# Kernel optimization log

Hardware: AMD Instinct MI355X
Metric: run time of the kernel (lower is better)

The kernel has to match this reference:

```python
import jax, jax.numpy as jnp
import numpy as np

S = 2048      # total tokens
DIM = 1024    # model dim
H = 16        # attention heads
DH = 64       # head dim
BOT = 256     # bottleneck dim
NIMG = 4      # images (equal size)
L = S // NIMG # tokens per image
K = 256       # sparse_k
IH = 4        # indexer heads
ID = 16       # indexer head dim
MAXREL = 64   # hardcoded in module
NBUCK = 2 * MAXREL + 1
GH = IH * 2   # gate MLP hidden (expansion=2)


def setup_inputs() -> dict:
    key = jax.random.key(0)
    ks = jax.random.split(key, 16)
    r = lambda i, sh, s=0.02: jax.random.normal(ks[i], sh, jnp.float32) * s
    return dict(
        hidden_states=jax.random.normal(ks[0], (S, DIM), jnp.float32),
        patch_coords=jax.random.randint(ks[1], (S, 2), 0, 64, dtype=jnp.int32),
        cu_seqlens=jnp.arange(NIMG + 1, dtype=jnp.int32) * L,
        rotary_pos_emb=jax.random.uniform(ks[2], (S, DH // 2), jnp.float32) * 3.0,
        Wq_idx=r(3, (2 * IH * ID, DIM)),
        Wk_idx=r(4, (2 * IH * ID, DIM)),
        W1g=r(5, (GH, IH)), b1g=jnp.zeros((GH,), jnp.float32),
        W2g=r(6, (IH, GH)), b2g=jnp.zeros((IH,), jnp.float32),
        rpe_table=r(7, (NBUCK, IH)),
        Wqkv_d=r(8, (BOT, DIM)), bqkv_d=jnp.zeros((BOT,), jnp.float32),
        Wqkv_u=r(9, (3 * DIM, BOT)), bqkv_u=jnp.zeros((3 * DIM,), jnp.float32),
        Wp_d=r(10, (BOT, DIM)), bp_d=jnp.zeros((BOT,), jnp.float32),
        Wp_u=r(11, (DIM, BOT)), bp_u=jnp.zeros((DIM,), jnp.float32),
        scaler=jnp.ones((1,), jnp.float32),
    )


def _rotate_half(x):
    x1, x2 = jnp.split(x, 2, axis=-1)
    return jnp.concatenate([-x2, x1], axis=-1)


def reference(hidden_states, patch_coords, cu_seqlens, rotary_pos_emb,
              Wq_idx, Wk_idx, W1g, b1g, W2g, b2g, rpe_table,
              Wqkv_d, bqkv_d, Wqkv_u, bqkv_u, Wp_d, bp_d, Wp_u, bp_u, scaler):
    n = cu_seqlens.shape[0] - 1            # images (equal size L)
    Li = hidden_states.shape[0] // n
    neg = jnp.finfo(hidden_states.dtype).min

    # QKV via low-rank bottleneck
    qkv = (hidden_states @ Wqkv_d.T + bqkv_d) @ Wqkv_u.T + bqkv_u  # [S, 3*DIM]
    qkv = qkv.reshape(S, 3, H, DH)
    q, k, v = qkv[:, 0], qkv[:, 1], qkv[:, 2]                      # [S, H, DH]

    # vision RoPE (emb = cat(rpe, rpe))
    emb = jnp.concatenate([rotary_pos_emb, rotary_pos_emb], axis=-1)  # [S, DH]
    cos = jnp.cos(emb)[:, None, :]
    sin = jnpp if False else jnp.sin(emb)[:, None, :]
    q = q * cos + _rotate_half(q) * sin
    k = k * cos + _rotate_half(k) * sin

    # ---- interaction indexer, vmapped over equal-size images ----
    xs = hidden_states.reshape(n, Li, DIM)
    pos = patch_coords[:, 1].reshape(n, Li).astype(jnp.float32)
    qI = (xs @ Wq_idx.T).reshape(n, Li, 2 * IH, ID)
    kI = (xs @ Wk_idx.T).reshape(n, Li, 2 * IH, ID)
    dot = jnp.einsum('nqhd,nkhd->nqkh', qI, kI)                    # [n, L, L, 2*IH]
    data_in, gate_in = dot[..., :IH], dot[..., IH:]
    rel = jnp.clip(pos[:, :, None] - pos[:, None, :], -MAXREL, MAXREL)
    bucket = (rel + MAXREL).astype(jnp.int32)                      # [n, L, L]
    rpe = rpe_table[bucket]                                        # [n, L, L, IH]
    relu_scores = jax.nn.relu(data_in + rpe)
    g = jax.nn.sigmoid(jax.nn.relu((gate_in + rpe) @ W1g.T + b1g) @ W2g.T + b2g)
    index_scores = (relu_scores * g).sum(-1)                       # [n, L, L]

    # top-k sparse mask (0 at selected keys, -inf-ish elsewhere)
    _, topk_idx = jax.lax.top_k(index_scores, K)                   # [n, L, K]
    ni = jnp.arange(n)[:, None, None]
    ri = jnp.arange(Li)[None, :, None]
    mask_local = jnp.full((n, Li, Li), neg, hidden_states.dtype).at[ni, ri, topk_idx].set(0.0)

    # block-diagonal full mask
    mask = jnp.full((S, S), neg, hidden_states.dtype)
    for i in range(n):
        mask = mask.at[i * Li:(i + 1) * Li, i * Li:(i + 1) * Li].set(mask_local[i])

    # dense SDPA with additive mask
    att = jnp.einsum('qhd,khd->hqk', q, k) / jnp.sqrt(jnp.float32(DH)).astype(q.dtype)
    att = att + mask[None]
    p = jax.nn.softmax(att, axis=-1)
    out = jnp.einsum('hqk,khd->qhd', p, v).reshape(S, H * DH)

    final = (out @ Wp_d.T + bp_d) @ Wp_u.T + bp_u
    return final * scaler
```

## Files before the change

### kernel.cpp

```cpp
#include <hip/hip_runtime.h>
#include <hip/hip_bf16.h>

#define S_    2048
#define DIM_  1024
#define H_    16
#define DH_   64
#define BOT_  256
#define NIMG_ 4
#define LI_   512
#define K_    256
#define IH_   4
#define ID_   16
#define MAXREL_ 64
#define NBUCK_ 129
#define GH_   8
#define IDH2_ 128

typedef short bf16x8 __attribute__((ext_vector_type(8)));
typedef float f32x4  __attribute__((ext_vector_type(4)));

__device__ __forceinline__ unsigned short f2bf(float x) {
    unsigned u = __float_as_uint(x);
    return (unsigned short)((u + 0x7fffu + ((u >> 16) & 1u)) >> 16);
}
__device__ __forceinline__ float bf2f(unsigned short h) {
    return __uint_as_float(((unsigned)h) << 16);
}

#define OFF_W1_    2097152
#define OFF_WQ_    2359296
#define OFF_WK_    2490368
#define OFF_WQKVU_ 2621440
#define OFF_WPD_   3407872
#define OFF_WPU_   3670016
#define NSPLIT_    3932160

__global__ __launch_bounds__(256) void split_all_kernel(
    const float* __restrict__ hid, const float* __restrict__ wqd,
    const float* __restrict__ wq,  const float* __restrict__ wk,
    const float* __restrict__ wqu, const float* __restrict__ wpd,
    const float* __restrict__ wpu,
    unsigned short* __restrict__ hi, unsigned short* __restrict__ lo)
{
    long e = ((long)blockIdx.x * 256 + threadIdx.x) * 4;
    if (e >= NSPLIT_) return;
    const float* src; long off;
    if (e < OFF_W1_)         { src = hid; off = 0; }
    else if (e < OFF_WQ_)    { src = wqd; off = OFF_W1_; }
    else if (e < OFF_WK_)    { src = wq;  off = OFF_WQ_; }
    else if (e < OFF_WQKVU_) { src = wk;  off = OFF_WK_; }
    else if (e < OFF_WPD_)   { src = wqu; off = OFF_WQKVU_; }
    else if (e < OFF_WPU_)   { src = wpd; off = OFF_WPD_; }
    else                     { src = wpu; off = OFF_WPU_; }
    float4 v = *(const float4*)(src + (e - off));
    ushort4 h, l;
    h.x = f2bf(v.x); l.x = f2bf(v.x - bf2f(h.x));
    h.y = f2bf(v.y); l.y = f2bf(v.y - bf2f(h.y));
    h.z = f2bf(v.z); l.z = f2bf(v.z - bf2f(h.z));
    h.w = f2bf(v.w); l.w = f2bf(v.w - bf2f(h.w));
    *(ushort4*)&hi[e] = h;
    *(ushort4*)&lo[e] = l;
}

__global__ __launch_bounds__(256) void gemm_bf16x3(
    const unsigned short* __restrict__ Ah, const unsigned short* __restrict__ Al,
    const unsigned short* __restrict__ Bh, const unsigned short* __restrict__ Bl,
    const float* __restrict__ bias, const float* __restrict__ scale_ptr,
    float* __restrict__ Cf, int M, int N, int Kd)
{
    __shared__ unsigned short sAh[128 * 40], sAl[128 * 40];
    __shared__ unsigned short sBh[64 * 40],  sBl[64 * 40];
    int tid = threadIdx.x;
    int lane = tid & 63, wv = tid >> 6;
    int wr = wv >> 1, wc = wv & 1;
    int row0 = blockIdx.y * 128, col0 = blockIdx.x * 64;

    f32x4 acc[4][2];
#pragma unroll
    for (int i = 0; i < 4; i++)
#pragma unroll
        for (int j = 0; j < 2; j++) acc[i][j] = (f32x4){0.f, 0.f, 0.f, 0.f};

    int ar = tid >> 1, ac = (tid & 1) * 16;
    int br = tid >> 2, bc = (tid & 3) * 8;
    const unsigned short* gAh = Ah + (size_t)(row0 + ar) * Kd + ac;
    const unsigned short* gAl = Al + (size_t)(row0 + ar) * Kd + ac;
    const unsigned short* gBh = Bh + (size_t)(col0 + br) * Kd + bc;
    const unsigned short* gBl = Bl + (size_t)(col0 + br) * Kd + bc;
    int am = lane & 15, qk = (lane >> 4) * 8;

    for (int k0 = 0; k0 < Kd; k0 += 32) {
        __syncthreads();
        *(float4*)&sAh[ar * 40 + ac]     = *(const float4*)(gAh + k0);
        *(float4*)&sAh[ar * 40 + ac + 8] = *(const float4*)(gAh + k0 + 8);
        *(float4*)&sAl[ar * 40 + ac]     = *(const float4*)(gAl + k0);
        *(float4*)&sAl[ar * 40 + ac + 8] = *(const float4*)(gAl + k0 + 8);
        *(float4*)&sBh[br * 40 + bc]     = *(const float4*)(gBh + k0);
        *(float4*)&sBl[br * 40 + bc]     = *(const float4*)(gBl + k0);
        __syncthreads();

        bf16x8 ah[4], al[4], bh[2], bl[2];
#pragma unroll
        for (int rt = 0; rt < 4; rt++) {
            int r = wr * 64 + rt * 16 + am;
            ah[rt] = *(const bf16x8*)&sAh[r * 40 + qk];
            al[rt] = *(const bf16x8*)&sAl[r * 40 + qk];
        }
#pragma unroll
        for (int ct = 0; ct < 2; ct++) {
            int c = wc * 32 + ct * 16 + am;
            bh[ct] = *(const bf16x8*)&sBh[c * 40 + qk];
            bl[ct] = *(const bf16x8*)&sBl[c * 40 + qk];
        }
#pragma unroll
        for (int rt = 0; rt < 4; rt++)
#pragma unroll
            for (int ct = 0; ct < 2; ct++) {
                acc[rt][ct] = __builtin_amdgcn_mfma_f32_16x16x32_bf16(ah[rt], bh[ct], acc[rt][ct], 0, 0, 0);
                acc[rt][ct] = __builtin_amdgcn_mfma_f32_16x16x32_bf16(ah[rt], bl[ct], acc[rt][ct], 0, 0, 0);
                acc[rt][ct] = __builtin_amdgcn_mfma_f32_16x16x32_bf16(al[rt], bh[ct], acc[rt][ct], 0, 0, 0);
            }
    }

    float scl = scale_ptr ? *scale_ptr : 1.0f;
    int rq = (lane >> 4) * 4;
#pragma unroll
    for (int rt = 0; rt < 4; rt++)
#pragma unroll
        for (int ct = 0; ct < 2; ct++) {
            int col = col0 + wc * 32 + ct * 16 + am;
            float bz = bias ? bias[col] : 0.0f;
#pragma unroll
            for (int rg = 0; rg < 4; rg++) {
                int row = row0 + wr * 64 + rt * 16 + rq + rg;
                Cf[(size_t)row * N + col] = (acc[rt][ct][rg] + bz) * scl;
            }
        }
}

__global__ __launch_bounds__(256) void gemm64_bf16x3(
    const unsigned short* __restrict__ Ah, const unsigned short* __restrict__ Al,
    const unsigned short* __restrict__ Bh, const unsigned short* __restrict__ Bl,
    const float* __restrict__ bias_lo, const float* __restrict__ bias_hi,
    float* __restrict__ Cf, unsigned short* __restrict__ Chi,
    unsigned short* __restrict__ Clo, int M, int N, int Kd, int split_col)
{
    __shared__ unsigned short sAh[64 * 72], sAl[64 * 72];
    __shared__ unsigned short sBh[64 * 72], sBl[64 * 72];
    int tid = threadIdx.x;
    int lane = tid & 63, wv = tid >> 6;
    int wr = wv >> 1, wc = wv & 1;
    int row0 = blockIdx.y * 64, col0 = blockIdx.x * 64;

    f32x4 acc[2][2];
#pragma unroll
    for (int i = 0; i < 2; i++)
#pragma unroll
        for (int j = 0; j < 2; j++) acc[i][j] = (f32x4){0.f, 0.f, 0.f, 0.f};

    int sr = tid >> 2, sc = (tid & 3) * 16;
    const unsigned short* gAh = Ah + (size_t)(row0 + sr) * Kd + sc;
    const unsigned short* gAl = Al + (size_t)(row0 + sr) * Kd + sc;
    const unsigned short* gBh = Bh + (size_t)(col0 + sr) * Kd + sc;
    const unsigned short* gBl = Bl + (size_t)(col0 + sr) * Kd + sc;
    int am = lane & 15, qk = (lane >> 4) * 8;

    for (int k0 = 0; k0 < Kd; k0 += 64) {
        __syncthreads();
        *(float4*)&sAh[sr * 72 + sc]     = *(const float4*)(gAh + k0);
        *(float4*)&sAh[sr * 72 + sc + 8] = *(const float4*)(gAh + k0 + 8);
        *(float4*)&sAl[sr * 72 + sc]     = *(const float4*)(gAl + k0);
        *(float4*)&sAl[sr * 72 + sc + 8] = *(const float4*)(gAl + k0 + 8);
        *(float4*)&sBh[sr * 72 + sc]     = *(const float4*)(gBh + k0);
        *(float4*)&sBh[sr * 72 + sc + 8] = *(const float4*)(gBh + k0 + 8);
        *(float4*)&sBl[sr * 72 + sc]     = *(const float4*)(gBl + k0);
        *(float4*)&sBl[sr * 72 + sc + 8] = *(const float4*)(gBl + k0 + 8);
        __syncthreads();

#pragma unroll
        for (int ks = 0; ks < 2; ks++) {
            bf16x8 ah[2], al[2], bh[2], bl[2];
#pragma unroll
            for (int rt = 0; rt < 2; rt++) {
                int r = wr * 32 + rt * 16 + am;
                ah[rt] = *(const bf16x8*)&sAh[r * 72 + ks * 32 + qk];
                al[rt] = *(const bf16x8*)&sAl[r * 72 + ks * 32 + qk];
            }
#pragma unroll
            for (int ct = 0; ct < 2; ct++) {
                int c = wc * 32 + ct * 16 + am;
                bh[ct] = *(const bf16x8*)&sBh[c * 72 + ks * 32 + qk];
                bl[ct] = *(const bf16x8*)&sBl[c * 72 + ks * 32 + qk];
            }
#pragma unroll
            for (int rt = 0; rt < 2; rt++)
#pragma unroll
                for (int ct = 0; ct < 2; ct++) {
                    acc[rt][ct] = __builtin_amdgcn_mfma_f32_16x16x32_bf16(ah[rt], bh[ct], acc[rt][ct], 0, 0, 0);
                    acc[rt][ct] = __builtin_amdgcn_mfma_f32_16x16x32_bf16(ah[rt], bl[ct], acc[rt][ct], 0, 0, 0);
                    acc[rt][ct] = __builtin_amdgcn_mfma_f32_16x16x32_bf16(al[rt], bh[ct], acc[rt][ct], 0, 0, 0);
                }
        }
    }

    int rq = (lane >> 4) * 4;
#pragma unroll
    for (int rt = 0; rt < 2; rt++)
#pragma unroll
        for (int ct = 0; ct < 2; ct++) {
            int col = col0 + wc * 32 + ct * 16 + am;
#pragma unroll
            for (int rg = 0; rg < 4; rg++) {
                int row = row0 + wr * 32 + rt * 16 + rq + rg;
                float v = acc[rt][ct][rg];
                if (col < split_col) {
                    if (bias_lo) v += bias_lo[col];
                    size_t idx = (size_t)row * split_col + col;
                    unsigned short hh = f2bf(v);
                    Chi[idx] = hh;
                    Clo[idx] = f2bf(v - bf2f(hh));
                } else {
                    if (bias_hi) v += bias_hi[col - split_col];
                    Cf[(size_t)row * (N - split_col) + col - split_col] = v;
                }
            }
        }
}

__global__ __launch_bounds__(256) void rope_kernel(
    float* __restrict__ qkv, const float* __restrict__ rope)
{
    int idx = blockIdx.x * blockDim.x + threadIdx.x;
    if (idx >= S_ * H_ * 32) return;
    int d = idx & 31;
    int h = (idx >> 5) & (H_ - 1);
    int s = idx >> 9;
    float r = rope[s * 32 + d];
    float c = cosf(r), sn = sinf(r);
    size_t base = (size_t)s * 3072 + h * 64 + d;
    float q1 = qkv[base], q2 = qkv[base + 32];
    qkv[base]      = q1 * c - q2 * sn;
    qkv[base + 32] = q2 * c + q1 * sn;
    float k1 = qkv[base + 1024], k2 = qkv[base + 1024 + 32];
    qkv[base + 1024]      = k1 * c - k2 * sn;
    qkv[base + 1024 + 32] = k2 * c + k1 * sn;
}

__global__ __launch_bounds__(256) void score_topk_kernel(
    const float* __restrict__ qIk,
    const int* __restrict__ coords, const float* __restrict__ rpe_table,
    const float* __restrict__ W1g, const float* __restrict__ b1g,
    const float* __restrict__ W2g, const float* __restrict__ b2g,
    unsigned* __restrict__ selmask)
{
    __shared__ float skI[64][132];
    __shared__ float sqI2[4][IDH2_];
    __shared__ unsigned skeys[4][LI_];
    __shared__ int shist[4][256];
    __shared__ float srpe[NBUCK_ * IH_];
    __shared__ float sW1[GH_ * IH_], sb1[GH_], sW2[IH_ * GH_], sb2[IH_];

    int tid  = threadIdx.x;
    int lane = tid & 63;
    int wv   = tid >> 6;
    int row  = blockIdx.x * 4 + wv;
    int n    = (blockIdx.x * 4) >> 9;

    for (int i = tid; i < NBUCK_ * IH_; i += 256) srpe[i] = rpe_table[i];
    if (tid < 32) sW1[tid] = W1g[tid];
    else if (tid < 64) sW2[tid - 32] = W2g[tid - 32];
    else if (tid < 72) sb1[tid - 64] = b1g[tid - 64];
    else if (tid < 76) sb2[tid - 72] = b2g[tid - 72];
    for (int i = tid; i < 4 * IDH2_; i += 256)
        sqI2[i >> 7][i & 127] =
            qIk[(size_t)(blockIdx.x * 4 + (i >> 7)) * 256 + (i & 127)];
    int pq = coords[row * 2 + 1];

    for (int kt = 0; kt < 8; kt++) {
        __syncthreads();
        {
            int r  = tid >> 2;
            int d0 = (tid & 3) * 32;
            const float* src = qIk + (size_t)(n * LI_ + kt * 64 + r) * 256 + 128 + d0;
#pragma unroll
            for (int j = 0; j < 8; j++)
                *(float4*)&skI[r][d0 + j * 4] = *(const float4*)(src + j * 4);
        }
        __syncthreads();

        int kloc = lane;
        int kg   = kt * 64 + kloc;
        const float* sq = &sqI2[wv][0];
        float dh[8];
#pragma unroll
        for (int hh = 0; hh < 8; hh++) {
            float acc = 0.0f;
#pragma unroll
            for (int d = 0; d < 16; d += 4) {
                float4 kv = *(const float4*)&skI[kloc][hh * 16 + d];
                acc += sq[hh * 16 + d + 0] * kv.x + sq[hh * 16 + d + 1] * kv.y +
                       sq[hh * 16 + d + 2] * kv.z + sq[hh * 16 + d + 3] * kv.w;
            }
            dh[hh] = acc;
        }
        int pk = coords[(n * LI_ + kg) * 2 + 1];
        int rel = pq - pk;
        rel = rel < -MAXREL_ ? -MAXREL_ : (rel > MAXREL_ ? MAXREL_ : rel);
        const float* rp = srpe + (rel + MAXREL_) * IH_;
        float t1[GH_];
#pragma unroll
        for (int g = 0; g < GH_; g++) t1[g] = sb1[g];
#pragma unroll
        for (int j = 0; j < IH_; j++) {
            float gate = dh[IH_ + j] + rp[j];
#pragma unroll
            for (int g = 0; g < GH_; g++) t1[g] += gate * sW1[g * IH_ + j];
        }
#pragma unroll
        for (int g = 0; g < GH_; g++) t1[g] = fmaxf(t1[g], 0.0f);
        float score = 0.0f;
#pragma unroll
        for (int j = 0; j < IH_; j++) {
            float t2 = sb2[j];
#pragma unroll
            for (int g = 0; g < GH_; g++) t2 += t1[g] * sW2[j * GH_ + g];
            float sg = 1.0f / (1.0f + expf(-t2));
            float rs = fmaxf(dh[j] + rp[j], 0.0f);
            score += rs * sg;
        }
        unsigned bits = __float_as_uint(score);
        skeys[wv][kg] = (bits & 0x80000000u) ? ~bits : (bits | 0x80000000u);
    }
    __syncthreads();

    unsigned pref = 0u;
    int kcur = K_;
    const unsigned himask[4] = {0u, 0xFF000000u, 0xFFFF0000u, 0xFFFFFF00u};
#pragma unroll
    for (int pass = 0; pass < 4; pass++) {
        int shift = 24 - pass * 8;
        unsigned hm = himask[pass];
        *(int4*)&shist[wv][4 * lane] = make_int4(0, 0, 0, 0);
        __syncthreads();
#pragma unroll
        for (int c = 0; c < 8; c++) {
            unsigned key = skeys[wv][c * 64 + lane];
            if ((key & hm) == pref) atomicAdd(&shist[wv][(key >> shift) & 255], 1);
        }
        __syncthreads();
        int4 b4 = *(const int4*)&shist[wv][4 * lane];
        int b[4] = {b4.x, b4.y, b4.z, b4.w};
        int t = b[0] + b[1] + b[2] + b[3];
        int Ssum = t;
#pragma unroll
        for (int off = 1; off < 64; off <<= 1) {
            int u = __shfl_down(Ssum, off, 64);
            if (lane + off < 64) Ssum += u;
        }
        int E = Ssum - t;
        int cs[5];
        cs[4] = E;
        cs[3] = b[3] + E;
        cs[2] = b[2] + cs[3];
        cs[1] = b[1] + cs[2];
        cs[0] = b[0] + cs[1];
        bool found = false;
        unsigned cpref = 0u; int ck = 0;
#pragma unroll
        for (int j = 0; j < 4; j++) {
            if (!found && cs[j] >= kcur && cs[j + 1] < kcur) {
                found = true;
                cpref = pref | ((unsigned)(4 * lane + j) << shift);
                ck = kcur - cs[j + 1];
            }
        }
        unsigned long long bm = __ballot(found);
        int src = __ffsll((long long)bm) - 1;
        pref = (unsigned)__shfl((int)cpref, src, 64);
        kcur = __shfl(ck, src, 64);
        __syncthreads();
    }
    unsigned Tu = pref;

    unsigned long long bg[8], be[8];
#pragma unroll
    for (int c = 0; c < 8; c++) {
        unsigned key = skeys[wv][c * 64 + lane];
        bg[c] = __ballot(key > Tu);
        be[c] = __ballot(key == Tu);
    }
    if (lane < 16) {
        int total_gt = 0;
#pragma unroll
        for (int c = 0; c < 8; c++) total_gt += __popcll(bg[c]);
        int base = 0;
#pragma unroll
        for (int c = 0; c < 8; c++) {
            if (2 * c < lane)     base += __popc((unsigned)be[c]);
            if (2 * c + 1 < lane) base += __popc((unsigned)(be[c] >> 32));
        }
        unsigned gw = (unsigned)(bg[lane >> 1] >> (32 * (lane & 1)));
        unsigned ew = (unsigned)(be[lane >> 1] >> (32 * (lane & 1)));
        int ne = K_ - total_gt - base;
        int pc = __popc(ew);
        int m = ne < 0 ? 0 : (ne > pc ? pc : ne);
        while (pc > m) { ew ^= (1u << (31 - __clz(ew))); pc--; }
        selmask[(size_t)row * 16 + lane] = gw | ew;
    }
}

__global__ __launch_bounds__(256) void attn_kernel(
    const float* __restrict__ qkv, const unsigned* __restrict__ selmask,
    unsigned short* __restrict__ outh, unsigned short* __restrict__ outl)
{
    __shared__ unsigned short Qh[64 * 72],  Ql[64 * 72];
    __shared__ unsigned short KPh[64 * 72], KPl[64 * 72];
    __shared__ unsigned short VTh[64 * 72], VTl[64 * 72];
    __shared__ unsigned Ms[64][16];

    int b  = blockIdx.x;
    int qt = b >> 6;
    int nh = b & 63;
    int h  = nh & 15;
    int n  = nh >> 4;
    int tid = threadIdx.x;
    int lane = tid & 63, w = tid >> 6;
    int lane15 = lane & 15, quad = lane >> 4;
    int q0 = n * LI_ + qt * 64;

    for (int i = tid; i < 64 * 16; i += 256)
        Ms[i >> 4][i & 15] = selmask[(size_t)(q0 + (i >> 4)) * 16 + (i & 15)];

    {
        int r = tid >> 2, c0 = (tid & 3) * 16;
        const float* src = qkv + (size_t)(q0 + r) * 3072 + h * 64 + c0;
        unsigned short hb[16], lb[16];
#pragma unroll
        for (int j = 0; j < 16; j += 4) {
            float4 v = *(const float4*)(src + j);
            float f[4] = {v.x * 0.125f, v.y * 0.125f, v.z * 0.125f, v.w * 0.125f};
#pragma unroll
            for (int t = 0; t < 4; t++) {
                unsigned short hh = f2bf(f[t]);
                hb[j + t] = hh;
                lb[j + t] = f2bf(f[t] - bf2f(hh));
            }
        }
        *(uint4*)&Qh[r * 72 + c0]     = *(uint4*)&hb[0];
        *(uint4*)&Qh[r * 72 + c0 + 8] = *(uint4*)&hb[8];
        *(uint4*)&Ql[r * 72 + c0]     = *(uint4*)&lb[0];
        *(uint4*)&Ql[r * 72 + c0 + 8] = *(uint4*)&lb[8];
    }

    f32x4 o_acc[4];
#pragma unroll
    for (int i = 0; i < 4; i++) o_acc[i] = (f32x4){0.f, 0.f, 0.f, 0.f};
    float rsum[4] = {};

    for (int kt = 0; kt < 8; kt++) {
        __syncthreads();
        {
            int r = tid >> 2, c0 = (tid & 3) * 16;
            const float* src = qkv + (size_t)(n * LI_ + kt * 64 + r) * 3072 + 1024 + h * 64 + c0;
            unsigned short hb[16], lb[16];
#pragma unroll
            for (int j = 0; j < 16; j += 4) {
                float4 v = *(const float4*)(src + j);
                float f[4] = {v.x, v.y, v.z, v.w};
#pragma unroll
                for (int t = 0; t < 4; t++) {
                    unsigned short hh = f2bf(f[t]);
                    hb[j + t] = hh;
                    lb[j + t] = f2bf(f[t] - bf2f(hh));
                }
            }
            *(uint4*)&KPh[r * 72 + c0]     = *(uint4*)&hb[0];
            *(uint4*)&KPh[r * 72 + c0 + 8] = *(uint4*)&hb[8];
            *(uint4*)&KPl[r * 72 + c0]     = *(uint4*)&lb[0];
            *(uint4*)&KPl[r * 72 + c0 + 8] = *(uint4*)&lb[8];
        }
        {
            int d = lane;
            int k0 = w * 16;
            const float* src = qkv + (size_t)(n * LI_ + kt * 64 + k0) * 3072 + 2048 + h * 64 + d;
            unsigned short hb[16], lb[16];
#pragma unroll
            for (int j = 0; j < 16; j++) {
                float f = src[(size_t)j * 3072];
                unsigned short hh = f2bf(f);
                hb[j] = hh;
                lb[j] = f2bf(f - bf2f(hh));
            }
            *(uint4*)&VTh[d * 72 + k0]     = *(uint4*)&hb[0];
            *(uint4*)&VTh[d * 72 + k0 + 8] = *(uint4*)&hb[8];
            *(uint4*)&VTl[d * 72 + k0]     = *(uint4*)&lb[0];
            *(uint4*)&VTl[d * 72 + k0 + 8] = *(uint4*)&lb[8];
        }
        __syncthreads();

        f32x4 s_acc[4];
#pragma unroll
        for (int nt = 0; nt < 4; nt++) s_acc[nt] = (f32x4){0.f, 0.f, 0.f, 0.f};
        {
            bf16x8 qfh[2], qfl[2];
#pragma unroll
            for (int ks = 0; ks < 2; ks++) {
                qfh[ks] = *(const bf16x8*)&Qh[(16 * w + lane15) * 72 + ks * 32 + quad * 8];
                qfl[ks] = *(const bf16x8*)&Ql[(16 * w + lane15) * 72 + ks * 32 + quad * 8];
            }
#pragma unroll
            for (int nt = 0; nt < 4; nt++) {
#pragma unroll
                for (int ks = 0; ks < 2; ks++) {
                    bf16x8 kfh = *(const bf16x8*)&KPh[(16 * nt + lane15) * 72 + ks * 32 + quad * 8];
                    bf16x8 kfl = *(const bf16x8*)&KPl[(16 * nt + lane15) * 72 + ks * 32 + quad * 8];
                    s_acc[nt] = __builtin_amdgcn_mfma_f32_16x16x32_bf16(qfh[ks], kfh, s_acc[nt], 0, 0, 0);
                    s_acc[nt] = __builtin_amdgcn_mfma_f32_16x16x32_bf16(qfh[ks], kfl, s_acc[nt], 0, 0, 0);
                    s_acc[nt] = __builtin_amdgcn_mfma_f32_16x16x32_bf16(qfl[ks], kfh, s_acc[nt], 0, 0, 0);
                }
            }
        }
        __syncthreads();

#pragma unroll
        for (int nt = 0; nt < 4; nt++) {
            int kb = kt * 64 + nt * 16 + lane15;
            int wi = kb >> 5, bit = kb & 31;
#pragma unroll
            for (int reg = 0; reg < 4; reg++) {
                int qloc = 16 * w + quad * 4 + reg;
                unsigned mw = Ms[qloc][wi];
                float p = ((mw >> bit) & 1u) ? __expf(s_acc[nt][reg]) : 0.0f;
                rsum[reg] += p;
                unsigned short ph = f2bf(p);
                KPh[qloc * 72 + nt * 16 + lane15] = ph;
                KPl[qloc * 72 + nt * 16 + lane15] = f2bf(p - bf2f(ph));
            }
        }
        __syncthreads();

        {
            bf16x8 pfh[2], pfl[2];
#pragma unroll
            for (int ks = 0; ks < 2; ks++) {
                pfh[ks] = *(const bf16x8*)&KPh[(16 * w + lane15) * 72 + ks * 32 + quad * 8];
                pfl[ks] = *(const bf16x8*)&KPl[(16 * w + lane15) * 72 + ks * 32 + quad * 8];
            }
#pragma unroll
            for (int dt = 0; dt < 4; dt++) {
#pragma unroll
                for (int ks = 0; ks < 2; ks++) {
                    bf16x8 vfh = *(const bf16x8*)&VTh[(16 * dt + lane15) * 72 + ks * 32 + quad * 8];
                    bf16x8 vfl = *(const bf16x8*)&VTl[(16 * dt + lane15) * 72 + ks * 32 + quad * 8];
                    o_acc[dt] = __builtin_amdgcn_mfma_f32_16x16x32_bf16(pfh[ks], vfh, o_acc[dt], 0, 0, 0);
                    o_acc[dt] = __builtin_amdgcn_mfma_f32_16x16x32_bf16(pfh[ks], vfl, o_acc[dt], 0, 0, 0);
                    o_acc[dt] = __builtin_amdgcn_mfma_f32_16x16x32_bf16(pfl[ks], vfh, o_acc[dt], 0, 0, 0);
                }
            }
        }
    }

#pragma unroll
    for (int reg = 0; reg < 4; reg++) {
        rsum[reg] += __shfl_xor(rsum[reg], 1, 64);
        rsum[reg] += __shfl_xor(rsum[reg], 2, 64);
        rsum[reg] += __shfl_xor(rsum[reg], 4, 64);
        rsum[reg] += __shfl_xor(rsum[reg], 8, 64);
    }

#pragma unroll
    for (int dt = 0; dt < 4; dt++) {
#pragma unroll
        for (int reg = 0; reg < 4; reg++) {
            float v = o_acc[dt][reg] / rsum[reg];
            size_t ob = (size_t)(q0 + 16 * w + quad * 4 + reg) * 1024 + h * 64 + 16 * dt + lane15;
            unsigned short hh = f2bf(v);
            outh[ob] = hh;
            outl[ob] = f2bf(v - bf2f(hh));
        }
    }
}

extern "C" void kernel_launch(void* const* d_in, const int* in_sizes, int n_in,
                              void* d_out, int out_size, void* d_ws, size_t ws_size,
                              hipStream_t stream)
{
    const float* hidden  = (const float*)d_in[0];
    const int*   coords  = (const int*)d_in[1];
    const float* rope    = (const float*)d_in[3];
    const float* Wq_idx  = (const float*)d_in[4];
    const float* Wk_idx  = (const float*)d_in[5];
    const float* W1g     = (const float*)d_in[6];
    const float* b1g     = (const float*)d_in[7];
    const float* W2g     = (const float*)d_in[8];
    const float* b2g     = (const float*)d_in[9];
    const float* rpe     = (const float*)d_in[10];
    const float* Wqkv_d  = (const float*)d_in[11];
    const float* bqkv_d  = (const float*)d_in[12];
    const float* Wqkv_u  = (const float*)d_in[13];
    const float* bqkv_u  = (const float*)d_in[14];
    const float* Wp_d    = (const float*)d_in[15];
    const float* bp_d    = (const float*)d_in[16];
    const float* Wp_u    = (const float*)d_in[17];
    const float* bp_u    = (const float*)d_in[18];
    const float* scaler  = (const float*)d_in[19];
    float* out = (float*)d_out;

    unsigned short* sp_hi  = (unsigned short*)d_ws;
    unsigned short* sp_lo  = sp_hi + NSPLIT_;
    unsigned short* mid_hi = sp_lo + NSPLIT_;
    unsigned short* mid_lo = mid_hi + (size_t)S_ * BOT_;
    float* qkv = (float*)(mid_lo + (size_t)S_ * BOT_);
    float* qIk = qkv + (size_t)S_ * 3 * DIM_;
    unsigned* selmask = (unsigned*)(qIk + (size_t)S_ * 256);

    split_all_kernel<<<(NSPLIT_ / 4 + 255) / 256, 256, 0, stream>>>(
        hidden, Wqkv_d, Wq_idx, Wk_idx, Wqkv_u, Wp_d, Wp_u, sp_hi, sp_lo);

    gemm64_bf16x3<<<dim3(512 / 64, S_ / 64), 256, 0, stream>>>(
        sp_hi, sp_lo, sp_hi + OFF_W1_, sp_lo + OFF_W1_,
        bqkv_d, nullptr, qIk, mid_hi, mid_lo, S_, 512, DIM_, 256);

    gemm_bf16x3<<<dim3(3 * DIM_ / 64, S_ / 128), 256, 0, stream>>>(
        mid_hi, mid_lo, sp_hi + OFF_WQKVU_, sp_lo + OFF_WQKVU_,
        bqkv_u, nullptr, qkv, S_, 3 * DIM_, BOT_);

    rope_kernel<<<(S_ * H_ * 32) / 256, 256, 0, stream>>>(qkv, rope);

    score_topk_kernel<<<S_ / 4, 256, 0, stream>>>(
        qIk, coords, rpe, W1g, b1g, W2g, b2g, selmask);

    attn_kernel<<<NIMG_ * H_ * 8, 256, 0, stream>>>(qkv, selmask, sp_hi, sp_lo);

    gemm64_bf16x3<<<dim3(BOT_ / 64, S_ / 64), 256, 0, stream>>>(
        sp_hi, sp_lo, sp_hi + OFF_WPD_, sp_lo + OFF_WPD_,
        bp_d, nullptr, nullptr, mid_hi, mid_lo, S_, BOT_, DIM_, BOT_);

    gemm_bf16x3<<<dim3(DIM_ / 64, S_ / 128), 256, 0, stream>>>(
        mid_hi, mid_lo, sp_hi + OFF_WPU_, sp_lo + OFF_WPU_,
        bp_u, scaler, out, S_, DIM_, BOT_);
}
```

Measured before the change: 251.4 us.

## Fuse RoPE with bf16 hi/lo split and decouple attention LDS buffers

The RoPE kernel now also applies the query scale and writes bf16 hi/lo split copies of Q, K and V once, so the attention kernel loads pre-split data instead of converting per block. This removes the conversion work that each of the 8 query-tile blocks redid for the same K and V. Attention gets separate K and P shared buffers, which lets it drop two barriers per key tile. The score kernel's LDS tile is XOR-swizzled instead of padded to avoid bank conflicts, and the score kernel is launched before the QKV up-projection. The cost is an extra split QKV buffer in workspace and more memory traffic in the RoPE pass.

```diff
diff --git a/kernel.cpp b/kernel.cpp
--- a/kernel.cpp
+++ b/kernel.cpp
@@ -227,23 +227,31 @@
         }
 }
 
-__global__ __launch_bounds__(256) void rope_kernel(
-    float* __restrict__ qkv, const float* __restrict__ rope)
+__global__ __launch_bounds__(256) void ropesplit_kernel(
+    const float* __restrict__ qkv, const float* __restrict__ rope,
+    unsigned short* __restrict__ qkvh, unsigned short* __restrict__ qkvl)
 {
-    int idx = blockIdx.x * blockDim.x + threadIdx.x;
-    if (idx >= S_ * H_ * 32) return;
-    int d = idx & 31;
-    int h = (idx >> 5) & (H_ - 1);
-    int s = idx >> 9;
-    float r = rope[s * 32 + d];
+    int idx = blockIdx.x * 256 + threadIdx.x;
+    int d = idx & 63;
+    int hh = (idx >> 6) & (H_ - 1);
+    int s = idx >> 10;
+    size_t base = (size_t)s * 3072 + hh * 64 + d;
+    float q = qkv[base];
+    float k = qkv[base + 1024];
+    float v = qkv[base + 2048];
+    float r = rope[s * 32 + (d & 31)];
     float c = cosf(r), sn = sinf(r);
-    size_t base = (size_t)s * 3072 + h * 64 + d;
-    float q1 = qkv[base], q2 = qkv[base + 32];
-    qkv[base]      = q1 * c - q2 * sn;
-    qkv[base + 32] = q2 * c + q1 * sn;
-    float k1 = qkv[base + 1024], k2 = qkv[base + 1024 + 32];
-    qkv[base + 1024]      = k1 * c - k2 * sn;
-    qkv[base + 1024 + 32] = k2 * c + k1 * sn;
+    float qp = __shfl_xor(q, 32, 64);
+    float kp = __shfl_xor(k, 32, 64);
+    float sgn = (d < 32) ? -1.0f : 1.0f;
+    float qr = (q * c + sgn * qp * sn) * 0.125f;
+    float kr = k * c + sgn * kp * sn;
+    unsigned short h1 = f2bf(qr);
+    qkvh[base] = h1;            qkvl[base] = f2bf(qr - bf2f(h1));
+    unsigned short h2 = f2bf(kr);
+    qkvh[base + 1024] = h2;     qkvl[base + 1024] = f2bf(kr - bf2f(h2));
+    unsigned short h3 = f2bf(v);
+    qkvh[base + 2048] = h3;     qkvl[base + 2048] = f2bf(v - bf2f(h3));
 }
 
 __global__ __launch_bounds__(256) void score_topk_kernel(
@@ -253,7 +261,7 @@
     const float* __restrict__ W2g, const float* __restrict__ b2g,
     unsigned* __restrict__ selmask)
 {
-    __shared__ float skI[64][132];
+    __shared__ float skI[64][128];
     __shared__ float sqI2[4][IDH2_];
     __shared__ unsigned skeys[4][LI_];
     __shared__ int shist[4][256];
@@ -282,24 +290,26 @@
             int r  = tid >> 2;
             int d0 = (tid & 3) * 32;
             const float* src = qIk + (size_t)(n * LI_ + kt * 64 + r) * 256 + 128 + d0;
+            int fb = d0 >> 2, sw = r & 7;
 #pragma unroll
             for (int j = 0; j < 8; j++)
-                *(float4*)&skI[r][d0 + j * 4] = *(const float4*)(src + j * 4);
+                *(float4*)&skI[r][((fb + j) ^ sw) << 2] = *(const float4*)(src + j * 4);
         }
         __syncthreads();
 
         int kloc = lane;
         int kg   = kt * 64 + kloc;
         const float* sq = &sqI2[wv][0];
+        int sw = kloc & 7;
         float dh[8];
 #pragma unroll
         for (int hh = 0; hh < 8; hh++) {
             float acc = 0.0f;
 #pragma unroll
-            for (int d = 0; d < 16; d += 4) {
-                float4 kv = *(const float4*)&skI[kloc][hh * 16 + d];
-                acc += sq[hh * 16 + d + 0] * kv.x + sq[hh * 16 + d + 1] * kv.y +
-                       sq[hh * 16 + d + 2] * kv.z + sq[hh * 16 + d + 3] * kv.w;
+            for (int dq = 0; dq < 4; dq++) {
+                float4 kv = *(const float4*)&skI[kloc][((hh * 4 + dq) ^ sw) << 2];
+                const float* sqp = sq + hh * 16 + dq * 4;
+                acc += sqp[0] * kv.x + sqp[1] * kv.y + sqp[2] * kv.z + sqp[3] * kv.w;
             }
             dh[hh] = acc;
         }
@@ -410,12 +420,14 @@
 }
 
 __global__ __launch_bounds__(256) void attn_kernel(
-    const float* __restrict__ qkv, const unsigned* __restrict__ selmask,
+    const unsigned short* __restrict__ qkvh, const unsigned short* __restrict__ qkvl,
+    const unsigned* __restrict__ selmask,
     unsigned short* __restrict__ outh, unsigned short* __restrict__ outl)
 {
     __shared__ unsigned short Qh[64 * 72],  Ql[64 * 72];
-    __shared__ unsigned short KPh[64 * 72], KPl[64 * 72];
+    __shared__ unsigned short Kh[64 * 72],  Kl[64 * 72];
     __shared__ unsigned short VTh[64 * 72], VTl[64 * 72];
+    __shared__ unsigned short Ph[64 * 72],  Pl[64 * 72];
     __shared__ unsigned Ms[64][16];
 
     int b  = blockIdx.x;
@@ -433,23 +445,11 @@
 
     {
         int r = tid >> 2, c0 = (tid & 3) * 16;
-        const float* src = qkv + (size_t)(q0 + r) * 3072 + h * 64 + c0;
-        unsigned short hb[16], lb[16];
-#pragma unroll
-        for (int j = 0; j < 16; j += 4) {
-            float4 v = *(const float4*)(src + j);
-            float f[4] = {v.x * 0.125f, v.y * 0.125f, v.z * 0.125f, v.w * 0.125f};
-#pragma unroll
-            for (int t = 0; t < 4; t++) {
-                unsigned short hh = f2bf(f[t]);
-                hb[j + t] = hh;
-                lb[j + t] = f2bf(f[t] - bf2f(hh));
-            }
-        }
-        *(uint4*)&Qh[r * 72 + c0]     = *(uint4*)&hb[0];
-        *(uint4*)&Qh[r * 72 + c0 + 8] = *(uint4*)&hb[8];
-        *(uint4*)&Ql[r * 72 + c0]     = *(uint4*)&lb[0];
-        *(uint4*)&Ql[r * 72 + c0 + 8] = *(uint4*)&lb[8];
+        size_t off = (size_t)(q0 + r) * 3072 + h * 64 + c0;
+        *(uint4*)&Qh[r * 72 + c0]     = *(const uint4*)(qkvh + off);
+        *(uint4*)&Qh[r * 72 + c0 + 8] = *(const uint4*)(qkvh + off + 8);
+        *(uint4*)&Ql[r * 72 + c0]     = *(const uint4*)(qkvl + off);
+        *(uint4*)&Ql[r * 72 + c0 + 8] = *(const uint4*)(qkvl + off + 8);
     }
 
     f32x4 o_acc[4];
@@ -461,40 +461,26 @@
         __syncthreads();
         {
             int r = tid >> 2, c0 = (tid & 3) * 16;
-            const float* src = qkv + (size_t)(n * LI_ + kt * 64 + r) * 3072 + 1024 + h * 64 + c0;
+            size_t off = (size_t)(n * LI_ + kt * 64 + r) * 3072 + 1024 + h * 64 + c0;
+            *(uint4*)&Kh[r * 72 + c0]     = *(const uint4*)(qkvh + off);
+            *(uint4*)&Kh[r * 72 + c0 + 8] = *(const uint4*)(qkvh + off + 8);
+            *(uint4*)&Kl[r * 72 + c0]     = *(const uint4*)(qkvl + off);
+            *(uint4*)&Kl[r * 72 + c0 + 8] = *(const uint4*)(qkvl + off + 8);
+        }
+        {
+            int dd = lane;
+            int k0 = w * 16;
+            size_t off = (size_t)(n * LI_ + kt * 64 + k0) * 3072 + 2048 + h * 64 + dd;
             unsigned short hb[16], lb[16];
 #pragma unroll
-            for (int j = 0; j < 16; j += 4) {
-                float4 v = *(const float4*)(src + j);
-                float f[4] = {v.x, v.y, v.z, v.w};
-#pragma unroll
-                for (int t = 0; t < 4; t++) {
-                    unsigned short hh = f2bf(f[t]);
-                    hb[j + t] = hh;
-                    lb[j + t] = f2bf(f[t] - bf2f(hh));
-                }
-            }
-            *(uint4*)&KPh[r * 72 + c0]     = *(uint4*)&hb[0];
-            *(uint4*)&KPh[r * 72 + c0 + 8] = *(uint4*)&hb[8];
-            *(uint4*)&KPl[r * 72 + c0]     = *(uint4*)&lb[0];
-            *(uint4*)&KPl[r * 72 + c0 + 8] = *(uint4*)&lb[8];
-        }
-        {
-            int d = lane;
-            int k0 = w * 16;
-            const float* src = qkv + (size_t)(n * LI_ + kt * 64 + k0) * 3072 + 2048 + h * 64 + d;
-            unsigned short hb[16], lb[16];
-#pragma unroll
             for (int j = 0; j < 16; j++) {
-                float f = src[(size_t)j * 3072];
-                unsigned short hh = f2bf(f);
-                hb[j] = hh;
-                lb[j] = f2bf(f - bf2f(hh));
-            }
-            *(uint4*)&VTh[d * 72 + k0]     = *(uint4*)&hb[0];
-            *(uint4*)&VTh[d * 72 + k0 + 8] = *(uint4*)&hb[8];
-            *(uint4*)&VTl[d * 72 + k0]     = *(uint4*)&lb[0];
-            *(uint4*)&VTl[d * 72 + k0 + 8] = *(uint4*)&lb[8];
+                hb[j] = qkvh[off + (size_t)j * 3072];
+                lb[j] = qkvl[off + (size_t)j * 3072];
+            }
+            *(uint4*)&VTh[dd * 72 + k0]     = *(uint4*)&hb[0];
+            *(uint4*)&VTh[dd * 72 + k0 + 8] = *(uint4*)&hb[8];
+            *(uint4*)&VTl[dd * 72 + k0]     = *(uint4*)&lb[0];
+            *(uint4*)&VTl[dd * 72 + k0 + 8] = *(uint4*)&lb[8];
         }
         __syncthreads();
 
@@ -512,15 +498,14 @@
             for (int nt = 0; nt < 4; nt++) {
 #pragma unroll
                 for (int ks = 0; ks < 2; ks++) {
-                    bf16x8 kfh = *(const bf16x8*)&KPh[(16 * nt + lane15) * 72 + ks * 32 + quad * 8];
-                    bf16x8 kfl = *(const bf16x8*)&KPl[(16 * nt + lane15) * 72 + ks * 32 + quad * 8];
+                    bf16x8 kfh = *(const bf16x8*)&Kh[(16 * nt + lane15) * 72 + ks * 32 + quad * 8];
+                    bf16x8 kfl = *(const bf16x8*)&Kl[(16 * nt + lane15) * 72 + ks * 32 + quad * 8];
                     s_acc[nt] = __builtin_amdgcn_mfma_f32_16x16x32_bf16(qfh[ks], kfh, s_acc[nt], 0, 0, 0);
                     s_acc[nt] = __builtin_amdgcn_mfma_f32_16x16x32_bf16(qfh[ks], kfl, s_acc[nt], 0, 0, 0);
                     s_acc[nt] = __builtin_amdgcn_mfma_f32_16x16x32_bf16(qfl[ks], kfh, s_acc[nt], 0, 0, 0);
                 }
             }
         }
-        __syncthreads();
 
 #pragma unroll
         for (int nt = 0; nt < 4; nt++) {
@@ -533,18 +518,17 @@
                 float p = ((mw >> bit) & 1u) ? __expf(s_acc[nt][reg]) : 0.0f;
                 rsum[reg] += p;
                 unsigned short ph = f2bf(p);
-                KPh[qloc * 72 + nt * 16 + lane15] = ph;
-                KPl[qloc * 72 + nt * 16 + lane15] = f2bf(p - bf2f(ph));
-            }
-        }
-        __syncthreads();
+                Ph[qloc * 72 + nt * 16 + lane15] = ph;
+                Pl[qloc * 72 + nt * 16 + lane15] = f2bf(p - bf2f(ph));
+            }
+        }
 
         {
             bf16x8 pfh[2], pfl[2];
 #pragma unroll
             for (int ks = 0; ks < 2; ks++) {
-                pfh[ks] = *(const bf16x8*)&KPh[(16 * w + lane15) * 72 + ks * 32 + quad * 8];
-                pfl[ks] = *(const bf16x8*)&KPl[(16 * w + lane15) * 72 + ks * 32 + quad * 8];
+                pfh[ks] = *(const bf16x8*)&Ph[(16 * w + lane15) * 72 + ks * 32 + quad * 8];
+                pfl[ks] = *(const bf16x8*)&Pl[(16 * w + lane15) * 72 + ks * 32 + quad * 8];
             }
 #pragma unroll
             for (int dt = 0; dt < 4; dt++) {
@@ -613,6 +597,8 @@
     float* qkv = (float*)(mid_lo + (size_t)S_ * BOT_);
     float* qIk = qkv + (size_t)S_ * 3 * DIM_;
     unsigned* selmask = (unsigned*)(qIk + (size_t)S_ * 256);
+    unsigned short* qkvh = (unsigned short*)(selmask + (size_t)S_ * 16);
+    unsigned short* qkvl = qkvh + (size_t)S_ * 3 * DIM_;
 
     split_all_kernel<<<(NSPLIT_ / 4 + 255) / 256, 256, 0, stream>>>(
         hidden, Wqkv_d, Wq_idx, Wk_idx, Wqkv_u, Wp_d, Wp_u, sp_hi, sp_lo);
@@ -621,16 +607,17 @@
         sp_hi, sp_lo, sp_hi + OFF_W1_, sp_lo + OFF_W1_,
         bqkv_d, nullptr, qIk, mid_hi, mid_lo, S_, 512, DIM_, 256);
 
+    score_topk_kernel<<<S_ / 4, 256, 0, stream>>>(
+        qIk, coords, rpe, W1g, b1g, W2g, b2g, selmask);
+
     gemm_bf16x3<<<dim3(3 * DIM_ / 64, S_ / 128), 256, 0, stream>>>(
         mid_hi, mid_lo, sp_hi + OFF_WQKVU_, sp_lo + OFF_WQKVU_,
         bqkv_u, nullptr, qkv, S_, 3 * DIM_, BOT_);
 
-    rope_kernel<<<(S_ * H_ * 32) / 256, 256, 0, stream>>>(qkv, rope);
-
-    score_topk_kernel<<<S_ / 4, 256, 0, stream>>>(
-        qIk, coords, rpe, W1g, b1g, W2g, b2g, selmask);
-
-    attn_kernel<<<NIMG_ * H_ * 8, 256, 0, stream>>>(qkv, selmask, sp_hi, sp_lo);
+    ropesplit_kernel<<<(S_ * H_ * 64) / 256, 256, 0, stream>>>(
+        qkv, rope, qkvh, qkvl);
+
+    attn_kernel<<<NIMG_ * H_ * 8, 256, 0, stream>>>(qkvh, qkvl, selmask, sp_hi, sp_lo);
 
     gemm64_bf16x3<<<dim3(BOT_ / 64, S_ / 64), 256, 0, stream>>>(
         sp_hi, sp_lo, sp_hi + OFF_WPD_, sp_lo + OFF_WPD_,
```

Result: slower. 270.0 us (+7.4%).
